# Performance work log

Measured on AMD Instinct MI355X. Metric: run time of the kernel, lower is better.

The kernel has to match this reference:

```python
import jax, jax.numpy as jnp
import numpy as np

B, Lq, C = 2, 4096, 768
H, W = 64, 64                 # single feature level, Lin = H*W = 4096
NH, NL, NP = 6, 1, 4          # heads, levels, sampling points
HD = C // NH                  # 128 per-head dim (deform_ratio = 1.0)
EPS = 1e-6
INIT_VALUES = 0.01


def _ln(x, w, b):
    m = jnp.mean(x, axis=-1, keepdims=True)
    xc = x - m
    v = jnp.mean(xc * xc, axis=-1, keepdims=True)
    return xc * jax.lax.rsqrt(v + EPS) * w + b


def _bilinear_gather(v, px, py, h, w):
    # v: [B,NH,h*w,HD]; px,py: [B,NH,Lq,NP] pixel coords (align_corners=False,
    # zero padding) -- matches F.grid_sample used by the pytorch fallback and
    # the Deformable-DETR CUDA kernel.
    x0 = jnp.floor(px); y0 = jnp.floor(py)
    fx = px - x0;       fy = py - y0
    x0i = x0.astype(jnp.int32); y0i = y0.astype(jnp.int32)
    out = 0.
    for dy, dx, wt in ((0, 0, (1 - fy) * (1 - fx)),
                       (0, 1, (1 - fy) * fx),
                       (1, 0, fy * (1 - fx)),
                       (1, 1, fy * fx)):
        yi = y0i + dy; xi = x0i + dx
        valid = ((yi >= 0) & (yi < h) & (xi >= 0) & (xi < w)).astype(v.dtype)
        idx = jnp.clip(yi, 0, h - 1) * w + jnp.clip(xi, 0, w - 1)  # [B,NH,Lq,NP]
        g = jnp.take_along_axis(v, idx.reshape(idx.shape[0], idx.shape[1], -1, 1), axis=2)
        g = g.reshape(idx.shape + (v.shape[-1],))                  # [B,NH,Lq,NP,HD]
        out = out + g * (wt * valid)[..., None]
    return out


def _ms_deform_attn_core(value, sampling_locations, attention_weights):
    # value [B,H*W,NH,HD]; locations [B,Lq,NH,NL,NP,2] in [0,1]; weights [B,Lq,NH,NL,NP]
    v = value.transpose(0, 2, 1, 3)                                 # [B,NH,HW,HD]
    loc = sampling_locations[:, :, :, 0].transpose(0, 2, 1, 3, 4)   # level 0: [B,NH,Lq,NP,2]
    px = loc[..., 0] * W - 0.5
    py = loc[..., 1] * H - 0.5
    sampled = _bilinear_gather(v, px, py, H, W)                     # [B,NH,Lq,NP,HD]
    aw = attention_weights[:, :, :, 0].transpose(0, 2, 1, 3)        # [B,NH,Lq,NP]
    out = jnp.einsum('bhqpd,bhqp->bqhd', sampled, aw)
    return out.reshape(B, Lq, NH * HD)


def setup_inputs() -> dict:
    key = jax.random.key(0)
    k = jax.random.split(key, 8)
    s = 0.02
    return {
        'x': jax.random.normal(k[0], (B, Lq, C), jnp.float32),
        'reference_points': jax.random.uniform(k[1], (B, Lq, NL, 2), jnp.float32),
        'feat': jax.random.normal(k[2], (B, H * W, C), jnp.float32),
        'spatial_shapes': jnp.array([[H, W]], jnp.int32),
        'level_start_index': jnp.zeros((1,), jnp.int32),
        'qn_w': jnp.ones((C,), jnp.float32),
        'qn_b': jnp.zeros((C,), jnp.float32),
        'fn_w': jnp.ones((C,), jnp.float32),
        'fn_b': jnp.zeros((C,), jnp.float32),
        'gamma': jnp.full((C,), INIT_VALUES, jnp.float32),
        'w_value': jax.random.normal(k[3], (C, C), jnp.float32) * s,
        'b_value': jnp.zeros((C,), jnp.float32),
        'w_off': jax.random.normal(k[4], (C, NH * NL * NP * 2), jnp.float32) * s,
        'b_off': jax.random.uniform(k[5], (NH * NL * NP * 2,), jnp.float32, -2.0, 2.0),
        'w_attn': jax.random.normal(k[6], (C, NH * NL * NP), jnp.float32) * s,
        'b_attn': jnp.zeros((NH * NL * NP,), jnp.float32),
        'w_out': jax.random.normal(k[7], (C, C), jnp.float32) * s,
        'b_out': jnp.zeros((C,), jnp.float32),
    }


def reference(x, reference_points, feat, spatial_shapes, level_start_index,
              qn_w, qn_b, fn_w, fn_b, gamma,
              w_value, b_value, w_off, b_off, w_attn, b_attn, w_out, b_out):
    q = _ln(x, qn_w, qn_b)
    f = _ln(feat, fn_w, fn_b)
    value = (f @ w_value + b_value).reshape(B, H * W, NH, HD)
    off = (q @ w_off + b_off).reshape(B, Lq, NH, NL, NP, 2)
    aw = (q @ w_attn + b_attn).reshape(B, Lq, NH, NL * NP)
    aw = jax.nn.softmax(aw, axis=-1).reshape(B, Lq, NH, NL, NP)
    # offset_normalizer = (W_l, H_l) per level
    norm = jnp.array([W, H], dtype=x.dtype)
    loc = reference_points[:, :, None, :, None, :] + off / norm    # [B,Lq,NH,NL,NP,2]
    attn = _ms_deform_attn_core(value, loc, aw)
    attn = attn @ w_out + b_out
    return x + gamma * attn
```

## Files before the change

kernel.cpp:

```cpp
#include <hip/hip_runtime.h>
#include <cstdint>
#include <cstddef>

#define GLOBAL_AS __attribute__((address_space(1)))
#define LDS_AS __attribute__((address_space(3)))

typedef unsigned short u16;
typedef unsigned int u32;
typedef __bf16 bf16x8 __attribute__((ext_vector_type(8)));
typedef float f32x4 __attribute__((ext_vector_type(4)));

static constexpr int CDIM = 768;
static constexpr int NROWS = 8192;
static constexpr int KS1 = 4;

__device__ __forceinline__ u16 f2bf(float f) {
  union { float f; u32 u; } v; v.f = f;
  return (u16)((v.u + 0x7fffu + ((v.u >> 16) & 1u)) >> 16);
}
__device__ __forceinline__ float bf2f(u16 h) {
  union { u32 u; float f; } v; v.u = ((u32)h) << 16;
  return v.f;
}
__device__ __forceinline__ float ldf(const void* p, size_t i, int F) {
  return F ? ((const float*)p)[i] : bf2f(((const u16*)p)[i]);
}
__device__ __forceinline__ void load_lds16(const u16* g, u16* l) {
  __builtin_amdgcn_global_load_lds((const GLOBAL_AS u32*)g, (LDS_AS u32*)l, 16, 0, 0);
}

__global__ __launch_bounds__(256) void detect_kernel(const u16* __restrict__ x, int* __restrict__ flag) {
  int t = threadIdx.x;
  int cnt = 0;
  for (int i = t; i < 16384; i += 256) {
    u16 v = x[i];
    if ((v & 0x7F80u) == 0x7F80u) cnt++;
  }
  #pragma unroll
  for (int m = 32; m >= 1; m >>= 1) cnt += __shfl_xor(cnt, m, 64);
  __shared__ int r[4];
  if ((t & 63) == 0) r[t >> 6] = cnt;
  __syncthreads();
  if (t == 0) flag[0] = (r[0] + r[1] + r[2] + r[3] > 4) ? 1 : 0;
}

__global__ __launch_bounds__(192) void ln_kernel(
    const void* __restrict__ x, const void* __restrict__ feat,
    const void* __restrict__ qw, const void* __restrict__ qb,
    const void* __restrict__ fw, const void* __restrict__ fb,
    u16* __restrict__ qout, u16* __restrict__ fout, const int* __restrict__ flagp) {
  const int F = *flagp;
  int row = blockIdx.x;
  const void *src, *w, *b; u16* dst; size_t base;
  if (row < NROWS) { src = x; base = (size_t)row*CDIM; w = qw; b = qb; dst = qout + base; }
  else { int r2 = row - NROWS; src = feat; base = (size_t)r2*CDIM; w = fw; b = fb; dst = fout + (size_t)r2*CDIM; }
  int t = threadIdx.x;
  float v[4];
  if (F) {
    float4 q = ((const float4*)((const float*)src + base))[t];
    v[0]=q.x; v[1]=q.y; v[2]=q.z; v[3]=q.w;
  } else {
    const u16* sp = (const u16*)src + base + t*4;
    v[0]=bf2f(sp[0]); v[1]=bf2f(sp[1]); v[2]=bf2f(sp[2]); v[3]=bf2f(sp[3]);
  }
  float s = v[0]+v[1]+v[2]+v[3];
  float sq = v[0]*v[0]+v[1]*v[1]+v[2]*v[2]+v[3]*v[3];
  #pragma unroll
  for (int m = 32; m >= 1; m >>= 1) { s += __shfl_xor(s, m, 64); sq += __shfl_xor(sq, m, 64); }
  __shared__ float red[6];
  int lane = t & 63, wv = t >> 6;
  if (lane == 0) { red[wv] = s; red[wv+3] = sq; }
  __syncthreads();
  s  = red[0]+red[1]+red[2];
  sq = red[3]+red[4]+red[5];
  float mean = s * (1.f/768.f);
  float var  = fmaxf(sq * (1.f/768.f) - mean*mean, 0.f);
  float inv  = rsqrtf(var + 1e-6f);
  u16 o[4];
  #pragma unroll
  for (int k = 0; k < 4; ++k) {
    float wk = ldf(w, t*4+k, F), bk = ldf(b, t*4+k, F);
    o[k] = f2bf((v[k]-mean)*inv*wk + bk);
  }
  *(ushort4*)(dst + t*4) = make_ushort4(o[0], o[1], o[2], o[3]);
}

__global__ __launch_bounds__(256) void prep_kernel(
    const void* __restrict__ wv_, const void* __restrict__ wo_,
    const void* __restrict__ woff, const void* __restrict__ wattn,
    u16* __restrict__ wvT, u16* __restrict__ woT, u16* __restrict__ woaT,
    const int* __restrict__ flagp) {
  const int F = *flagp;
  if (blockIdx.z == 2) {
    int idx = (blockIdx.y * 24 + blockIdx.x) * 256 + threadIdx.x;
    if (idx >= 128 * CDIM) return;
    int n = idx / CDIM, k = idx - n*CDIM;
    float v = 0.f;
    if (n < 48)      v = ldf(woff, (size_t)k*48 + n, F);
    else if (n < 72) v = ldf(wattn, (size_t)k*24 + (n-48), F);
    woaT[idx] = f2bf(v);
    return;
  }
  __shared__ u16 tile[32][33];
  const void* in = blockIdx.z ? wo_ : wv_;
  u16* out       = blockIdx.z ? woT : wvT;
  int bn = blockIdx.x * 32;
  int bk = blockIdx.y * 32;
  int tx = threadIdx.x & 31, ty = threadIdx.x >> 5;
  #pragma unroll
  for (int i = ty; i < 32; i += 8)
    tile[i][tx] = F ? f2bf(((const float*)in)[(size_t)(bk+i)*CDIM + bn + tx])
                    : ((const u16*)in)[(size_t)(bk+i)*CDIM + bn + tx];
  __syncthreads();
  #pragma unroll
  for (int i = ty; i < 32; i += 8)
    out[(size_t)(bn+i)*CDIM + bk + tx] = tile[tx][i];
}

template<int EPI>
__global__ __launch_bounds__(256) void gemm_bt(
    const u16* __restrict__ A, const u16* __restrict__ Bt, void* __restrict__ Cout,
    const void* __restrict__ bias0, const void* __restrict__ bias1,
    const void* __restrict__ xres, const void* __restrict__ gammap,
    const int* __restrict__ flagp) {
  const int F = *flagp;
  __shared__ __align__(16) u16 smem[12288];
  u16* As = smem;
  u16* Bs = smem + 8192;
  u16* Cs = smem;
  const int m0 = blockIdx.x * 128;
  const int n0 = blockIdx.y * 64;
  const int t = threadIdx.x, lane = t & 63, wv = t >> 6;
  const int wm = wv & 1, wn = wv >> 1;
  const int kChunk = CDIM / gridDim.z;
  const int kbase = blockIdx.z * kChunk;
  const int lrow = lane >> 2;
  const int lcol = (lane & 3) * 8;
  f32x4 acc[4][2] = {};

  for (int k0 = kbase; k0 < kbase + kChunk; k0 += 64) {
    #pragma unroll
    for (int j = 0; j < 4; ++j) {
      int g = wv*4 + j;
      int p = g >> 3, s = g & 7;
      load_lds16(A + (size_t)(m0 + s*16 + lrow)*CDIM + k0 + p*32 + lcol,
                 As + p*4096 + s*512);
    }
    #pragma unroll
    for (int j = 0; j < 2; ++j) {
      int g = wv*2 + j;
      int p = g >> 2, s = g & 3;
      load_lds16(Bt + (size_t)(n0 + s*16 + lrow)*CDIM + k0 + p*32 + lcol,
                 Bs + p*2048 + s*512);
    }
    __syncthreads();
    #pragma unroll
    for (int u = 0; u < 2; ++u) {
      bf16x8 af[4], bfr[2];
      const int kc = (lane >> 4) * 8;
      #pragma unroll
      for (int i = 0; i < 4; ++i)
        af[i]  = *(const bf16x8*)(As + u*4096 + (wm*64 + i*16 + (lane & 15))*32 + kc);
      #pragma unroll
      for (int j = 0; j < 2; ++j)
        bfr[j] = *(const bf16x8*)(Bs + u*2048 + (wn*32 + j*16 + (lane & 15))*32 + kc);
      #pragma unroll
      for (int i = 0; i < 4; ++i)
        #pragma unroll
        for (int j = 0; j < 2; ++j)
          acc[i][j] = __builtin_amdgcn_mfma_f32_16x16x32_bf16(af[i], bfr[j], acc[i][j], 0, 0, 0);
    }
    __syncthreads();
  }

  const int r0 = (lane >> 4) * 4;
  const int c  = lane & 15;

  if (EPI == 1) {
    float* op = (float*)Cout + (size_t)blockIdx.z * NROWS * 72;
    #pragma unroll
    for (int i = 0; i < 4; ++i)
      #pragma unroll
      for (int j = 0; j < 2; ++j) {
        int col = n0 + wn*32 + j*16 + c;
        if (col < 72) {
          float bb = 0.f;
          if (blockIdx.z == 0) bb = (col < 48) ? ldf(bias0, col, F) : ldf(bias1, col-48, F);
          #pragma unroll
          for (int r = 0; r < 4; ++r)
            op[(size_t)(m0 + wm*64 + i*16 + r0 + r)*72 + col] = acc[i][j][r] + bb;
        }
      }
    return;
  }

  #pragma unroll
  for (int i = 0; i < 4; ++i)
    #pragma unroll
    for (int j = 0; j < 2; ++j) {
      int col = wn*32 + j*16 + c;
      float bb = ldf(bias0, n0 + col, F);
      #pragma unroll
      for (int r = 0; r < 4; ++r)
        Cs[(wm*64 + i*16 + r0 + r)*64 + col] = f2bf(acc[i][j][r] + bb);
    }
  __syncthreads();
  #pragma unroll
  for (int it = 0; it < 4; ++it) {
    int idx = it*256 + t;
    int row = idx >> 3, colb = (idx & 7) * 8;
    size_t gbase = (size_t)(m0 + row)*CDIM + n0 + colb;
    const u16* cp = Cs + row*64 + colb;
    if (EPI == 0) {
      *(bf16x8*)((u16*)Cout + gbase) = *(const bf16x8*)cp;
    } else {
      if (F) {
        const float* xp = (const float*)xres + gbase;
        const float* gp = (const float*)gammap + n0 + colb;
        float4 x0 = *(const float4*)xp,      x1 = *(const float4*)(xp + 4);
        float4 g0 = *(const float4*)gp,      g1 = *(const float4*)(gp + 4);
        float4 o0, o1;
        o0.x = x0.x + g0.x*bf2f(cp[0]); o0.y = x0.y + g0.y*bf2f(cp[1]);
        o0.z = x0.z + g0.z*bf2f(cp[2]); o0.w = x0.w + g0.w*bf2f(cp[3]);
        o1.x = x1.x + g1.x*bf2f(cp[4]); o1.y = x1.y + g1.y*bf2f(cp[5]);
        o1.z = x1.z + g1.z*bf2f(cp[6]); o1.w = x1.w + g1.w*bf2f(cp[7]);
        *(float4*)((float*)Cout + gbase)     = o0;
        *(float4*)((float*)Cout + gbase + 4) = o1;
      } else {
        const u16* xp = (const u16*)xres + gbase;
        const u16* gp = (const u16*)gammap + n0 + colb;
        u16 ov[8];
        #pragma unroll
        for (int k = 0; k < 8; ++k)
          ov[k] = f2bf(bf2f(xp[k]) + bf2f(gp[k]) * bf2f(cp[k]));
        *(bf16x8*)((u16*)Cout + gbase) = *(const bf16x8*)ov;
      }
    }
  }
}

__global__ __launch_bounds__(256) void sample_kernel(
    const u16* __restrict__ value,
    const float* __restrict__ offawp,
    const void* __restrict__ refp,
    u16* __restrict__ out, const int* __restrict__ flagp) {
  const int F = *flagp;
  const int wq   = blockIdx.x * 4 + (threadIdx.x >> 6);
  const int lane = threadIdx.x & 63;
  const int row  = wq / 3;
  const int h0   = (wq % 3) * 2;
  const int b    = row >> 12;
  const float* pr = offawp + (size_t)row*72;
  float rx = ldf(refp, (size_t)row*2,   F) * 64.f - 0.5f;
  float ry = ldf(refp, (size_t)row*2+1, F) * 64.f - 0.5f;

  float wts[2][16]; int offs[2][16];
  #pragma unroll
  for (int s = 0; s < 2; ++s) {
    const int h = h0 + s;
    float ob[8], aw4[4];
    #pragma unroll
    for (int k = 0; k < 8; ++k) {
      float v = 0.f;
      #pragma unroll
      for (int z = 0; z < KS1; ++z) v += pr[(size_t)z*NROWS*72 + h*8 + k];
      ob[k] = v;
    }
    #pragma unroll
    for (int k = 0; k < 4; ++k) {
      float v = 0.f;
      #pragma unroll
      for (int z = 0; z < KS1; ++z) v += pr[(size_t)z*NROWS*72 + 48 + h*4 + k];
      aw4[k] = v;
    }
    float mx = fmaxf(fmaxf(aw4[0],aw4[1]), fmaxf(aw4[2],aw4[3]));
    float e0 = __expf(aw4[0]-mx), e1 = __expf(aw4[1]-mx), e2 = __expf(aw4[2]-mx), e3 = __expf(aw4[3]-mx);
    float rs = 1.f / (e0+e1+e2+e3);
    float awt[4] = {e0*rs, e1*rs, e2*rs, e3*rs};
    #pragma unroll
    for (int p = 0; p < 4; ++p) {
      float px = rx + ob[p*2];
      float py = ry + ob[p*2+1];
      float x0f = floorf(px), y0f = floorf(py);
      float fx = px - x0f, fy = py - y0f;
      int x0 = (int)x0f, y0 = (int)y0f;
      #pragma unroll
      for (int dy = 0; dy < 2; ++dy)
        #pragma unroll
        for (int dx = 0; dx < 2; ++dx) {
          int yi = y0 + dy, xi = x0 + dx;
          bool valid = (yi >= 0) & (yi < 64) & (xi >= 0) & (xi < 64);
          float wt = (dy ? fy : 1.f-fy) * (dx ? fx : 1.f-fx) * awt[p];
          wts[s][p*4+dy*2+dx] = valid ? wt : 0.f;
          int yc = min(max(yi, 0), 63), xc = min(max(xi, 0), 63);
          offs[s][p*4+dy*2+dx] = (yc*64 + xc) * 384;
        }
    }
  }
  const u32* vbase = (const u32*)value + (size_t)b*4096*384 + h0*64 + lane;
  u32 vals[2][16];
  #pragma unroll
  for (int s = 0; s < 2; ++s)
    #pragma unroll
    for (int i = 0; i < 16; ++i)
      vals[s][i] = (vbase + s*64)[offs[s][i]];
  #pragma unroll
  for (int s = 0; s < 2; ++s) {
    float accx = 0.f, accy = 0.f;
    #pragma unroll
    for (int i = 0; i < 16; ++i) {
      accx += wts[s][i] * bf2f((u16)(vals[s][i] & 0xffffu));
      accy += wts[s][i] * bf2f((u16)(vals[s][i] >> 16));
    }
    ((u32*)out)[(size_t)row*384 + (h0+s)*64 + lane] = (u32)f2bf(accx) | ((u32)f2bf(accy) << 16);
  }
}

extern "C" void kernel_launch(void* const* d_in, const int* in_sizes, int n_in,
                              void* d_out, int out_size, void* d_ws, size_t ws_size,
                              hipStream_t stream) {
  const void* x       = d_in[0];
  const void* refp    = d_in[1];
  const void* feat    = d_in[2];
  const void* qn_w    = d_in[5];
  const void* qn_b    = d_in[6];
  const void* fn_w    = d_in[7];
  const void* fn_b    = d_in[8];
  const void* gamma   = d_in[9];
  const void* w_value = d_in[10];
  const void* b_value = d_in[11];
  const void* w_off   = d_in[12];
  const void* b_off   = d_in[13];
  const void* w_attn  = d_in[14];
  const void* b_attn  = d_in[15];
  const void* w_out   = d_in[16];
  const void* b_out   = d_in[17];

  char* p = (char*)d_ws;
  const size_t act = (size_t)NROWS * CDIM * 2;
  u16* q_bf   = (u16*)p; p += act;
  u16* f_bf   = (u16*)p; p += act;
  u16* val_bf = (u16*)p; p += act;
  u16* wvT    = (u16*)p; p += (size_t)CDIM*CDIM*2;
  u16* woT    = (u16*)p; p += (size_t)CDIM*CDIM*2;
  u16* woaT   = (u16*)p; p += (size_t)128*CDIM*2;
  float* offawp = (float*)p; p += (size_t)KS1*NROWS*72*4;
  int* dflag  = (int*)p; p += 256;
  u16* samp_bf = q_bf;

  detect_kernel<<<dim3(1), 256, 0, stream>>>((const u16*)x, dflag);
  prep_kernel<<<dim3(24,24,3), 256, 0, stream>>>(w_value, w_out, w_off, w_attn, wvT, woT, woaT, dflag);
  ln_kernel<<<dim3(16384), 192, 0, stream>>>(x, feat, qn_w, qn_b, fn_w, fn_b, q_bf, f_bf, dflag);
  gemm_bt<0><<<dim3(64,12,1),   256, 0, stream>>>(f_bf, wvT, val_bf, b_value, nullptr, nullptr, nullptr, dflag);
  gemm_bt<1><<<dim3(64,2,KS1),  256, 0, stream>>>(q_bf, woaT, offawp, b_off, b_attn, nullptr, nullptr, dflag);
  sample_kernel<<<dim3(6144), 256, 0, stream>>>(val_bf, offawp, refp, samp_bf, dflag);
  gemm_bt<2><<<dim3(64,12,1),   256, 0, stream>>>(samp_bf, woT, d_out, b_out, nullptr, x, gamma, dflag);
}
```

Measured before the change: 232.8 us.

## Drop dtype detection, fuse prep/LN kernels and merge value/offset GEMMs

Removes the runtime dtype-detection kernel and all per-element float/bf16 branching, hard-coding fp32 inputs. The weight transpose/convert and both LayerNorms now run in one launch, and the value projection and split-K offset/attention projection run as one grid. This cuts the number of kernel launches from seven to four and removes serial dependencies on a single-block detect kernel. In exchange the code no longer supports bf16 inputs.

```diff
diff --git a/kernel.cpp b/kernel.cpp
--- a/kernel.cpp
+++ b/kernel.cpp
@@ -22,108 +22,180 @@
   union { u32 u; float f; } v; v.u = ((u32)h) << 16;
   return v.f;
 }
-__device__ __forceinline__ float ldf(const void* p, size_t i, int F) {
-  return F ? ((const float*)p)[i] : bf2f(((const u16*)p)[i]);
-}
 __device__ __forceinline__ void load_lds16(const u16* g, u16* l) {
   __builtin_amdgcn_global_load_lds((const GLOBAL_AS u32*)g, (LDS_AS u32*)l, 16, 0, 0);
 }
 
-__global__ __launch_bounds__(256) void detect_kernel(const u16* __restrict__ x, int* __restrict__ flag) {
-  int t = threadIdx.x;
-  int cnt = 0;
-  for (int i = t; i < 16384; i += 256) {
-    u16 v = x[i];
-    if ((v & 0x7F80u) == 0x7F80u) cnt++;
-  }
-  #pragma unroll
-  for (int m = 32; m >= 1; m >>= 1) cnt += __shfl_xor(cnt, m, 64);
-  __shared__ int r[4];
-  if ((t & 63) == 0) r[t >> 6] = cnt;
-  __syncthreads();
-  if (t == 0) flag[0] = (r[0] + r[1] + r[2] + r[3] > 4) ? 1 : 0;
-}
-
-__global__ __launch_bounds__(192) void ln_kernel(
-    const void* __restrict__ x, const void* __restrict__ feat,
-    const void* __restrict__ qw, const void* __restrict__ qb,
-    const void* __restrict__ fw, const void* __restrict__ fb,
-    u16* __restrict__ qout, u16* __restrict__ fout, const int* __restrict__ flagp) {
-  const int F = *flagp;
-  int row = blockIdx.x;
-  const void *src, *w, *b; u16* dst; size_t base;
-  if (row < NROWS) { src = x; base = (size_t)row*CDIM; w = qw; b = qb; dst = qout + base; }
-  else { int r2 = row - NROWS; src = feat; base = (size_t)r2*CDIM; w = fw; b = fb; dst = fout + (size_t)r2*CDIM; }
-  int t = threadIdx.x;
-  float v[4];
-  if (F) {
-    float4 q = ((const float4*)((const float*)src + base))[t];
-    v[0]=q.x; v[1]=q.y; v[2]=q.z; v[3]=q.w;
-  } else {
-    const u16* sp = (const u16*)src + base + t*4;
-    v[0]=bf2f(sp[0]); v[1]=bf2f(sp[1]); v[2]=bf2f(sp[2]); v[3]=bf2f(sp[3]);
-  }
-  float s = v[0]+v[1]+v[2]+v[3];
-  float sq = v[0]*v[0]+v[1]*v[1]+v[2]*v[2]+v[3]*v[3];
-  #pragma unroll
-  for (int m = 32; m >= 1; m >>= 1) { s += __shfl_xor(s, m, 64); sq += __shfl_xor(sq, m, 64); }
-  __shared__ float red[6];
-  int lane = t & 63, wv = t >> 6;
-  if (lane == 0) { red[wv] = s; red[wv+3] = sq; }
-  __syncthreads();
-  s  = red[0]+red[1]+red[2];
-  sq = red[3]+red[4]+red[5];
-  float mean = s * (1.f/768.f);
-  float var  = fmaxf(sq * (1.f/768.f) - mean*mean, 0.f);
-  float inv  = rsqrtf(var + 1e-6f);
-  u16 o[4];
-  #pragma unroll
-  for (int k = 0; k < 4; ++k) {
-    float wk = ldf(w, t*4+k, F), bk = ldf(b, t*4+k, F);
-    o[k] = f2bf((v[k]-mean)*inv*wk + bk);
-  }
-  *(ushort4*)(dst + t*4) = make_ushort4(o[0], o[1], o[2], o[3]);
-}
-
-__global__ __launch_bounds__(256) void prep_kernel(
-    const void* __restrict__ wv_, const void* __restrict__ wo_,
-    const void* __restrict__ woff, const void* __restrict__ wattn,
-    u16* __restrict__ wvT, u16* __restrict__ woT, u16* __restrict__ woaT,
-    const int* __restrict__ flagp) {
-  const int F = *flagp;
-  if (blockIdx.z == 2) {
-    int idx = (blockIdx.y * 24 + blockIdx.x) * 256 + threadIdx.x;
-    if (idx >= 128 * CDIM) return;
+__global__ __launch_bounds__(192) void pre_kernel(
+    const float* __restrict__ x, const float* __restrict__ feat,
+    const float* __restrict__ qw, const float* __restrict__ qb,
+    const float* __restrict__ fw, const float* __restrict__ fb,
+    const float* __restrict__ wv_, const float* __restrict__ wo_,
+    const float* __restrict__ woff, const float* __restrict__ wattn,
+    u16* __restrict__ qout, u16* __restrict__ fout,
+    u16* __restrict__ wvT, u16* __restrict__ woT, u16* __restrict__ woaT) {
+  __shared__ __align__(8) char shbuf[32*33*2];
+  const int bx = blockIdx.x;
+  const int t = threadIdx.x;
+  if (bx < 2*NROWS) {
+    const float *src, *w, *b; u16* dst; size_t base;
+    if (bx < NROWS) { src = x; base = (size_t)bx*CDIM; w = qw; b = qb; dst = qout + base; }
+    else { int r2 = bx - NROWS; src = feat; base = (size_t)r2*CDIM; w = fw; b = fb; dst = fout + (size_t)r2*CDIM; }
+    float4 q = ((const float4*)(src + base))[t];
+    float v[4] = {q.x, q.y, q.z, q.w};
+    float s = v[0]+v[1]+v[2]+v[3];
+    float sq = v[0]*v[0]+v[1]*v[1]+v[2]*v[2]+v[3]*v[3];
+    #pragma unroll
+    for (int m = 32; m >= 1; m >>= 1) { s += __shfl_xor(s, m, 64); sq += __shfl_xor(sq, m, 64); }
+    float* red = (float*)shbuf;
+    int lane = t & 63, wv = t >> 6;
+    if (lane == 0) { red[wv] = s; red[wv+3] = sq; }
+    __syncthreads();
+    s  = red[0]+red[1]+red[2];
+    sq = red[3]+red[4]+red[5];
+    float mean = s * (1.f/768.f);
+    float var  = fmaxf(sq * (1.f/768.f) - mean*mean, 0.f);
+    float inv  = rsqrtf(var + 1e-6f);
+    float4 wq_ = ((const float4*)w)[t];
+    float4 bq_ = ((const float4*)b)[t];
+    u16 o[4];
+    o[0] = f2bf((v[0]-mean)*inv*wq_.x + bq_.x);
+    o[1] = f2bf((v[1]-mean)*inv*wq_.y + bq_.y);
+    o[2] = f2bf((v[2]-mean)*inv*wq_.z + bq_.z);
+    o[3] = f2bf((v[3]-mean)*inv*wq_.w + bq_.w);
+    *(ushort4*)(dst + t*4) = make_ushort4(o[0], o[1], o[2], o[3]);
+    return;
+  }
+  const int pid = bx - 2*NROWS;
+  const int z   = pid / 576;
+  const int rem = pid - z*576;
+  if (z == 2) {
+    int idx = rem*192 + t;
+    if (idx >= 128*CDIM) return;
     int n = idx / CDIM, k = idx - n*CDIM;
     float v = 0.f;
-    if (n < 48)      v = ldf(woff, (size_t)k*48 + n, F);
-    else if (n < 72) v = ldf(wattn, (size_t)k*24 + (n-48), F);
+    if (n < 48)      v = woff[(size_t)k*48 + n];
+    else if (n < 72) v = wattn[(size_t)k*24 + (n-48)];
     woaT[idx] = f2bf(v);
     return;
   }
-  __shared__ u16 tile[32][33];
-  const void* in = blockIdx.z ? wo_ : wv_;
-  u16* out       = blockIdx.z ? woT : wvT;
-  int bn = blockIdx.x * 32;
-  int bk = blockIdx.y * 32;
-  int tx = threadIdx.x & 31, ty = threadIdx.x >> 5;
-  #pragma unroll
-  for (int i = ty; i < 32; i += 8)
-    tile[i][tx] = F ? f2bf(((const float*)in)[(size_t)(bk+i)*CDIM + bn + tx])
-                    : ((const u16*)in)[(size_t)(bk+i)*CDIM + bn + tx];
+  u16* tile = (u16*)shbuf;
+  const float* in = z ? wo_ : wv_;
+  u16* out        = z ? woT : wvT;
+  int bn = (rem % 24) * 32;
+  int bk = (rem / 24) * 32;
+  int tx = t & 31, ty = t >> 5;
+  for (int i = ty; i < 32; i += 6)
+    tile[i*33 + tx] = f2bf(in[(size_t)(bk+i)*CDIM + bn + tx]);
   __syncthreads();
-  #pragma unroll
-  for (int i = ty; i < 32; i += 8)
-    out[(size_t)(bn+i)*CDIM + bk + tx] = tile[tx][i];
-}
-
-template<int EPI>
-__global__ __launch_bounds__(256) void gemm_bt(
-    const u16* __restrict__ A, const u16* __restrict__ Bt, void* __restrict__ Cout,
-    const void* __restrict__ bias0, const void* __restrict__ bias1,
-    const void* __restrict__ xres, const void* __restrict__ gammap,
-    const int* __restrict__ flagp) {
-  const int F = *flagp;
+  for (int i = ty; i < 32; i += 6)
+    out[(size_t)(bn+i)*CDIM + bk + tx] = tile[tx*33 + i];
+}
+
+__global__ __launch_bounds__(256) void gemm01(
+    const u16* __restrict__ Af, const u16* __restrict__ Aq,
+    const u16* __restrict__ wvT, const u16* __restrict__ woaT,
+    u16* __restrict__ val_bf, float* __restrict__ offawp,
+    const float* __restrict__ b_value, const float* __restrict__ b_off,
+    const float* __restrict__ b_attn) {
+  __shared__ __align__(16) u16 smem[12288];
+  u16* As = smem;
+  u16* Bs = smem + 8192;
+  u16* Cs = smem;
+  const int m0 = blockIdx.x * 128;
+  const bool isVal = blockIdx.y < 12;
+  const int g  = blockIdx.y - 12;
+  const int n0 = isVal ? blockIdx.y * 64 : (g & 1) * 64;
+  const int zz = isVal ? 0 : (g >> 1);
+  const int kbase = isVal ? 0 : zz * (CDIM / KS1);
+  const int kend  = kbase + (isVal ? CDIM : CDIM / KS1);
+  const u16* A  = isVal ? Af : Aq;
+  const u16* Bt = isVal ? wvT : woaT;
+  const int t = threadIdx.x, lane = t & 63, wv = t >> 6;
+  const int wm = wv & 1, wn = wv >> 1;
+  const int lrow = lane >> 2;
+  const int lcol = (lane & 3) * 8;
+  f32x4 acc[4][2] = {};
+
+  for (int k0 = kbase; k0 < kend; k0 += 64) {
+    #pragma unroll
+    for (int j = 0; j < 4; ++j) {
+      int gg = wv*4 + j;
+      int p = gg >> 3, s = gg & 7;
+      load_lds16(A + (size_t)(m0 + s*16 + lrow)*CDIM + k0 + p*32 + lcol,
+                 As + p*4096 + s*512);
+    }
+    #pragma unroll
+    for (int j = 0; j < 2; ++j) {
+      int gg = wv*2 + j;
+      int p = gg >> 2, s = gg & 3;
+      load_lds16(Bt + (size_t)(n0 + s*16 + lrow)*CDIM + k0 + p*32 + lcol,
+                 Bs + p*2048 + s*512);
+    }
+    __syncthreads();
+    #pragma unroll
+    for (int u = 0; u < 2; ++u) {
+      bf16x8 af[4], bfr[2];
+      const int kc = (lane >> 4) * 8;
+      #pragma unroll
+      for (int i = 0; i < 4; ++i)
+        af[i]  = *(const bf16x8*)(As + u*4096 + (wm*64 + i*16 + (lane & 15))*32 + kc);
+      #pragma unroll
+      for (int j = 0; j < 2; ++j)
+        bfr[j] = *(const bf16x8*)(Bs + u*2048 + (wn*32 + j*16 + (lane & 15))*32 + kc);
+      #pragma unroll
+      for (int i = 0; i < 4; ++i)
+        #pragma unroll
+        for (int j = 0; j < 2; ++j)
+          acc[i][j] = __builtin_amdgcn_mfma_f32_16x16x32_bf16(af[i], bfr[j], acc[i][j], 0, 0, 0);
+    }
+    __syncthreads();
+  }
+
+  const int r0 = (lane >> 4) * 4;
+  const int c  = lane & 15;
+
+  if (!isVal) {
+    float* op = offawp + (size_t)zz * NROWS * 72;
+    #pragma unroll
+    for (int i = 0; i < 4; ++i)
+      #pragma unroll
+      for (int j = 0; j < 2; ++j) {
+        int col = n0 + wn*32 + j*16 + c;
+        if (col < 72) {
+          float bb = 0.f;
+          if (zz == 0) bb = (col < 48) ? b_off[col] : b_attn[col-48];
+          #pragma unroll
+          for (int r = 0; r < 4; ++r)
+            op[(size_t)(m0 + wm*64 + i*16 + r0 + r)*72 + col] = acc[i][j][r] + bb;
+        }
+      }
+    return;
+  }
+
+  #pragma unroll
+  for (int i = 0; i < 4; ++i)
+    #pragma unroll
+    for (int j = 0; j < 2; ++j) {
+      int col = wn*32 + j*16 + c;
+      float bb = b_value[n0 + col];
+      #pragma unroll
+      for (int r = 0; r < 4; ++r)
+        Cs[(wm*64 + i*16 + r0 + r)*64 + col] = f2bf(acc[i][j][r] + bb);
+    }
+  __syncthreads();
+  #pragma unroll
+  for (int it = 0; it < 4; ++it) {
+    int idx = it*256 + t;
+    int row = idx >> 3, colb = (idx & 7) * 8;
+    *(bf16x8*)(val_bf + (size_t)(m0 + row)*CDIM + n0 + colb) = *(const bf16x8*)(Cs + row*64 + colb);
+  }
+}
+
+__global__ __launch_bounds__(256) void gemm2(
+    const u16* __restrict__ A, const u16* __restrict__ Bt, float* __restrict__ Cout,
+    const float* __restrict__ bias0, const float* __restrict__ xres,
+    const float* __restrict__ gammap) {
   __shared__ __align__(16) u16 smem[12288];
   u16* As = smem;
   u16* Bs = smem + 8192;
@@ -132,24 +204,22 @@
   const int n0 = blockIdx.y * 64;
   const int t = threadIdx.x, lane = t & 63, wv = t >> 6;
   const int wm = wv & 1, wn = wv >> 1;
-  const int kChunk = CDIM / gridDim.z;
-  const int kbase = blockIdx.z * kChunk;
   const int lrow = lane >> 2;
   const int lcol = (lane & 3) * 8;
   f32x4 acc[4][2] = {};
 
-  for (int k0 = kbase; k0 < kbase + kChunk; k0 += 64) {
+  for (int k0 = 0; k0 < CDIM; k0 += 64) {
     #pragma unroll
     for (int j = 0; j < 4; ++j) {
-      int g = wv*4 + j;
-      int p = g >> 3, s = g & 7;
+      int gg = wv*4 + j;
+      int p = gg >> 3, s = gg & 7;
       load_lds16(A + (size_t)(m0 + s*16 + lrow)*CDIM + k0 + p*32 + lcol,
                  As + p*4096 + s*512);
     }
     #pragma unroll
     for (int j = 0; j < 2; ++j) {
-      int g = wv*2 + j;
-      int p = g >> 2, s = g & 3;
+      int gg = wv*2 + j;
+      int p = gg >> 2, s = gg & 3;
       load_lds16(Bt + (size_t)(n0 + s*16 + lrow)*CDIM + k0 + p*32 + lcol,
                  Bs + p*2048 + s*512);
     }
@@ -175,31 +245,12 @@
 
   const int r0 = (lane >> 4) * 4;
   const int c  = lane & 15;
-
-  if (EPI == 1) {
-    float* op = (float*)Cout + (size_t)blockIdx.z * NROWS * 72;
-    #pragma unroll
-    for (int i = 0; i < 4; ++i)
-      #pragma unroll
-      for (int j = 0; j < 2; ++j) {
-        int col = n0 + wn*32 + j*16 + c;
-        if (col < 72) {
-          float bb = 0.f;
-          if (blockIdx.z == 0) bb = (col < 48) ? ldf(bias0, col, F) : ldf(bias1, col-48, F);
-          #pragma unroll
-          for (int r = 0; r < 4; ++r)
-            op[(size_t)(m0 + wm*64 + i*16 + r0 + r)*72 + col] = acc[i][j][r] + bb;
-        }
-      }
-    return;
-  }
-
   #pragma unroll
   for (int i = 0; i < 4; ++i)
     #pragma unroll
     for (int j = 0; j < 2; ++j) {
       int col = wn*32 + j*16 + c;
-      float bb = ldf(bias0, n0 + col, F);
+      float bb = bias0[n0 + col];
       #pragma unroll
       for (int r = 0; r < 4; ++r)
         Cs[(wm*64 + i*16 + r0 + r)*64 + col] = f2bf(acc[i][j][r] + bb);
@@ -211,48 +262,33 @@
     int row = idx >> 3, colb = (idx & 7) * 8;
     size_t gbase = (size_t)(m0 + row)*CDIM + n0 + colb;
     const u16* cp = Cs + row*64 + colb;
-    if (EPI == 0) {
-      *(bf16x8*)((u16*)Cout + gbase) = *(const bf16x8*)cp;
-    } else {
-      if (F) {
-        const float* xp = (const float*)xres + gbase;
-        const float* gp = (const float*)gammap + n0 + colb;
-        float4 x0 = *(const float4*)xp,      x1 = *(const float4*)(xp + 4);
-        float4 g0 = *(const float4*)gp,      g1 = *(const float4*)(gp + 4);
-        float4 o0, o1;
-        o0.x = x0.x + g0.x*bf2f(cp[0]); o0.y = x0.y + g0.y*bf2f(cp[1]);
-        o0.z = x0.z + g0.z*bf2f(cp[2]); o0.w = x0.w + g0.w*bf2f(cp[3]);
-        o1.x = x1.x + g1.x*bf2f(cp[4]); o1.y = x1.y + g1.y*bf2f(cp[5]);
-        o1.z = x1.z + g1.z*bf2f(cp[6]); o1.w = x1.w + g1.w*bf2f(cp[7]);
-        *(float4*)((float*)Cout + gbase)     = o0;
-        *(float4*)((float*)Cout + gbase + 4) = o1;
-      } else {
-        const u16* xp = (const u16*)xres + gbase;
-        const u16* gp = (const u16*)gammap + n0 + colb;
-        u16 ov[8];
-        #pragma unroll
-        for (int k = 0; k < 8; ++k)
-          ov[k] = f2bf(bf2f(xp[k]) + bf2f(gp[k]) * bf2f(cp[k]));
-        *(bf16x8*)((u16*)Cout + gbase) = *(const bf16x8*)ov;
-      }
-    }
+    const float* xp = xres + gbase;
+    const float* gp = gammap + n0 + colb;
+    float4 x0 = *(const float4*)xp,  x1 = *(const float4*)(xp + 4);
+    float4 g0 = *(const float4*)gp,  g1 = *(const float4*)(gp + 4);
+    float4 o0, o1;
+    o0.x = x0.x + g0.x*bf2f(cp[0]); o0.y = x0.y + g0.y*bf2f(cp[1]);
+    o0.z = x0.z + g0.z*bf2f(cp[2]); o0.w = x0.w + g0.w*bf2f(cp[3]);
+    o1.x = x1.x + g1.x*bf2f(cp[4]); o1.y = x1.y + g1.y*bf2f(cp[5]);
+    o1.z = x1.z + g1.z*bf2f(cp[6]); o1.w = x1.w + g1.w*bf2f(cp[7]);
+    *(float4*)(Cout + gbase)     = o0;
+    *(float4*)(Cout + gbase + 4) = o1;
   }
 }
 
 __global__ __launch_bounds__(256) void sample_kernel(
     const u16* __restrict__ value,
     const float* __restrict__ offawp,
-    const void* __restrict__ refp,
-    u16* __restrict__ out, const int* __restrict__ flagp) {
-  const int F = *flagp;
+    const float* __restrict__ refp,
+    u16* __restrict__ out) {
   const int wq   = blockIdx.x * 4 + (threadIdx.x >> 6);
   const int lane = threadIdx.x & 63;
   const int row  = wq / 3;
   const int h0   = (wq % 3) * 2;
   const int b    = row >> 12;
   const float* pr = offawp + (size_t)row*72;
-  float rx = ldf(refp, (size_t)row*2,   F) * 64.f - 0.5f;
-  float ry = ldf(refp, (size_t)row*2+1, F) * 64.f - 0.5f;
+  float rx = refp[(size_t)row*2]   * 64.f - 0.5f;
+  float ry = refp[(size_t)row*2+1] * 64.f - 0.5f;
 
   float wts[2][16]; int offs[2][16];
   #pragma unroll
@@ -319,22 +355,22 @@
 extern "C" void kernel_launch(void* const* d_in, const int* in_sizes, int n_in,
                               void* d_out, int out_size, void* d_ws, size_t ws_size,
                               hipStream_t stream) {
-  const void* x       = d_in[0];
-  const void* refp    = d_in[1];
-  const void* feat    = d_in[2];
-  const void* qn_w    = d_in[5];
-  const void* qn_b    = d_in[6];
-  const void* fn_w    = d_in[7];
-  const void* fn_b    = d_in[8];
-  const void* gamma   = d_in[9];
-  const void* w_value = d_in[10];
-  const void* b_value = d_in[11];
-  const void* w_off   = d_in[12];
-  const void* b_off   = d_in[13];
-  const void* w_attn  = d_in[14];
-  const void* b_attn  = d_in[15];
-  const void* w_out   = d_in[16];
-  const void* b_out   = d_in[17];
+  const float* x       = (const float*)d_in[0];
+  const float* refp    = (const float*)d_in[1];
+  const float* feat    = (const float*)d_in[2];
+  const float* qn_w    = (const float*)d_in[5];
+  const float* qn_b    = (const float*)d_in[6];
+  const float* fn_w    = (const float*)d_in[7];
+  const float* fn_b    = (const float*)d_in[8];
+  const float* gamma   = (const float*)d_in[9];
+  const float* w_value = (const float*)d_in[10];
+  const float* b_value = (const float*)d_in[11];
+  const float* w_off   = (const float*)d_in[12];
+  const float* b_off   = (const float*)d_in[13];
+  const float* w_attn  = (const float*)d_in[14];
+  const float* b_attn  = (const float*)d_in[15];
+  const float* w_out   = (const float*)d_in[16];
+  const float* b_out   = (const float*)d_in[17];
 
   char* p = (char*)d_ws;
   const size_t act = (size_t)NROWS * CDIM * 2;
@@ -345,14 +381,13 @@
   u16* woT    = (u16*)p; p += (size_t)CDIM*CDIM*2;
   u16* woaT   = (u16*)p; p += (size_t)128*CDIM*2;
   float* offawp = (float*)p; p += (size_t)KS1*NROWS*72*4;
-  int* dflag  = (int*)p; p += 256;
   u16* samp_bf = q_bf;
 
-  detect_kernel<<<dim3(1), 256, 0, stream>>>((const u16*)x, dflag);
-  prep_kernel<<<dim3(24,24,3), 256, 0, stream>>>(w_value, w_out, w_off, w_attn, wvT, woT, woaT, dflag);
-  ln_kernel<<<dim3(16384), 192, 0, stream>>>(x, feat, qn_w, qn_b, fn_w, fn_b, q_bf, f_bf, dflag);
-  gemm_bt<0><<<dim3(64,12,1),   256, 0, stream>>>(f_bf, wvT, val_bf, b_value, nullptr, nullptr, nullptr, dflag);
-  gemm_bt<1><<<dim3(64,2,KS1),  256, 0, stream>>>(q_bf, woaT, offawp, b_off, b_attn, nullptr, nullptr, dflag);
-  sample_kernel<<<dim3(6144), 256, 0, stream>>>(val_bf, offawp, refp, samp_bf, dflag);
-  gemm_bt<2><<<dim3(64,12,1),   256, 0, stream>>>(samp_bf, woT, d_out, b_out, nullptr, x, gamma, dflag);
-}
+  pre_kernel<<<dim3(2*NROWS + 1728), 192, 0, stream>>>(
+      x, feat, qn_w, qn_b, fn_w, fn_b, w_value, w_out, w_off, w_attn,
+      q_bf, f_bf, wvT, woT, woaT);
+  gemm01<<<dim3(64, 20), 256, 0, stream>>>(
+      f_bf, q_bf, wvT, woaT, val_bf, offawp, b_value, b_off, b_attn);
+  sample_kernel<<<dim3(6144), 256, 0, stream>>>(val_bf, offawp, refp, samp_bf);
+  gemm2<<<dim3(64, 12), 256, 0, stream>>>(samp_bf, woT, (float*)d_out, b_out, x, gamma);
+}
```

After: 199.6 us. -14.3%, faster.
